# Optimization experiments

Hardware: AMD Instinct MI355X
Metric: run time of the kernel (lower is better)

## Reference

```python
import jax, jax.numpy as jnp
import numpy as np

DIM = 768
NUM_HEADS = 16
D_K = DIM // NUM_HEADS


def setup_inputs() -> dict:
    key = jax.random.key(0)
    ks = jax.random.split(key, 9)
    B, T = 4, 2048
    s = 1.0 / np.sqrt(DIM)
    return {
        "x": jax.random.normal(ks[0], (B, T, DIM), dtype=jnp.float32),
        "Wq": jax.random.normal(ks[1], (DIM, DIM), dtype=jnp.float32) * s,
        "bq": jnp.zeros((DIM,), dtype=jnp.float32),
        "Wk": jax.random.normal(ks[2], (DIM, DIM), dtype=jnp.float32) * s,
        "bk": jnp.zeros((DIM,), dtype=jnp.float32),
        "Wv": jax.random.normal(ks[3], (DIM, DIM), dtype=jnp.float32) * s,
        "bv": jnp.zeros((DIM,), dtype=jnp.float32),
        "Wp": jax.random.normal(ks[4], (DIM, DIM), dtype=jnp.float32) * s,
        "bp": jnp.zeros((DIM,), dtype=jnp.float32),
    }


def reference(x, Wq, bq, Wk, bk, Wv, bv, Wp, bp):
    B, T, _ = x.shape
    # QKV projections (weights stored as [in, out])
    q = x @ Wq + bq
    k = x @ Wk + bk
    v = x @ Wv + bv
    # split heads: (B, H, T, d_k)
    q = q.reshape(B, T, NUM_HEADS, D_K).transpose(0, 2, 1, 3)
    k = k.reshape(B, T, NUM_HEADS, D_K).transpose(0, 2, 1, 3)
    v = v.reshape(B, T, NUM_HEADS, D_K).transpose(0, 2, 1, 3)
    # scaled dot-product attention; dropout omitted (eval mode)
    scores = jnp.einsum("bhtd,bhsd->bhts", q, k) / jnp.sqrt(jnp.float32(D_K))
    attn = jax.nn.softmax(scores, axis=-1)
    out = jnp.einsum("bhts,bhsd->bhtd", attn, v)
    out = out.transpose(0, 2, 1, 3).reshape(B, T, DIM)
    return out @ Wp + bp
```

## Files before the change

kernel.cpp:

```cpp
#include <hip/hip_runtime.h>
#include <math.h>

#define T_SEQ 2048
#define B_SZ  4
#define DIM   768
#define NH    16
#define DK    48
#define NQK   1536
#define N3    2304

typedef __bf16 bf16x8 __attribute__((ext_vector_type(8)));
typedef float  f32x4  __attribute__((ext_vector_type(4)));

__device__ __forceinline__ unsigned short f32_to_bf16(float f) {
    unsigned u = __float_as_uint(f);
    u += 0x7FFFu + ((u >> 16) & 1u);
    return (unsigned short)(u >> 16);
}
__device__ __forceinline__ unsigned pack_bf16x2(float a, float b) {
    unsigned r;
    asm("v_cvt_pk_bf16_f32 %0, %1, %2" : "=v"(r) : "v"(a), "v"(b));
    return r;
}
__device__ __forceinline__ void lds_dma16(const unsigned short* g, unsigned short* l) {
    __builtin_amdgcn_global_load_lds(
        (const __attribute__((address_space(1))) unsigned int*)g,
        (__attribute__((address_space(3))) unsigned int*)l, 16, 0, 0);
}

__global__ __launch_bounds__(256) void cvt_x_kernel(
    const float* __restrict__ x, unsigned short* __restrict__ xb)
{
    int i = blockIdx.x * 256 + threadIdx.x;
    const float* p = x + (size_t)i * 8;
    float4 f0 = *(const float4*)p;
    float4 f1 = *(const float4*)(p + 4);
    uint4 u;
    u.x = pack_bf16x2(f0.x, f0.y);
    u.y = pack_bf16x2(f0.z, f0.w);
    u.z = pack_bf16x2(f1.x, f1.y);
    u.w = pack_bf16x2(f1.z, f1.w);
    *(uint4*)(xb + (size_t)i * 8) = u;
}

__global__ __launch_bounds__(256) void pack_w_kernel(
    const float* __restrict__ Wq, const float* __restrict__ Wk,
    const float* __restrict__ Wv, const float* __restrict__ Wp,
    unsigned short* __restrict__ Wt, unsigned short* __restrict__ Wpt,
    float qscale)
{
    __shared__ float T[32][33];
    const int mode = blockIdx.z;
    const float* W = (mode == 0) ? Wq : (mode == 1) ? Wk : (mode == 2) ? Wv : Wp;
    const float sc = (mode == 0) ? qscale : 1.0f;
    const int k0 = blockIdx.x * 32, c0 = blockIdx.y * 32;
    const int tx = threadIdx.x & 31, ty = threadIdx.x >> 5;

#pragma unroll
    for (int r = 0; r < 4; ++r) {
        int row = ty + r * 8;
        T[row][tx] = W[(size_t)(k0 + row) * DIM + c0 + tx];
    }
    __syncthreads();
#pragma unroll
    for (int r = 0; r < 4; ++r) {
        int j   = ty + r * 8;
        int col = c0 + j;
        int k   = k0 + tx;
        unsigned short v = f32_to_bf16(T[tx][j] * sc);
        if (mode < 3) Wt[(size_t)(mode * 768 + col) * DIM + k] = v;
        else          Wpt[(size_t)col * DIM + k] = v;
    }
}

__global__ __launch_bounds__(256) void pack_bias_kernel(
    const float* __restrict__ bq, const float* __restrict__ bk,
    const float* __restrict__ bv, float* __restrict__ b3, float qscale)
{
    int n = blockIdx.x * 256 + threadIdx.x;
    if (n >= N3) return;
    float v;
    if (n < 768)       v = bq[n] * qscale;
    else if (n < 1536) v = bk[n - 768];
    else               v = bv[n - 1536];
    b3[n] = v;
}

__global__ __launch_bounds__(256) void gemm_qkv_kernel(
    const unsigned short* __restrict__ A, const unsigned short* __restrict__ Bt,
    const float* __restrict__ bias, unsigned short* __restrict__ QK,
    unsigned short* __restrict__ vT)
{
    __shared__ __align__(16) unsigned short As[2 * 128 * 32];
    __shared__ __align__(16) unsigned short Bs[2 * 128 * 32];

    const int t = threadIdx.x;
    const int w = t >> 6, lane = t & 63, quad = lane >> 4, lr = lane & 15;
    const int wm = w >> 1, wn = w & 1;

    const int bid = blockIdx.x;
    const int gy8 = bid / 144;
    const int rem = bid - gy8 * 144;
    const int bx  = rem >> 3;
    const int by  = (rem & 7) | (gy8 << 3);
    const int m0 = by * 128, n0 = bx * 128;

    const int cw0 = w * 128, cw1 = w * 128 + 64;
    const int ca = cw0 + lane, cb = cw1 + lane;
    const int ra = ca >> 2, sa = (ca & 3) * 8;
    const int rb = cb >> 2, sb = (cb & 3) * 8;

    const unsigned short* Ara = A  + (size_t)(m0 + ra) * DIM + sa;
    const unsigned short* Arb = A  + (size_t)(m0 + rb) * DIM + sb;
    const unsigned short* Bra = Bt + (size_t)(n0 + ra) * DIM + sa;
    const unsigned short* Brb = Bt + (size_t)(n0 + rb) * DIM + sb;

    f32x4 acc[4][4] = {};

    lds_dma16(Ara, As + cw0 * 8);
    lds_dma16(Arb, As + cw1 * 8);
    lds_dma16(Bra, Bs + cw0 * 8);
    lds_dma16(Brb, Bs + cw1 * 8);
    __syncthreads();

    for (int k0 = 0; k0 < DIM; k0 += 32) {
        const int cur = (k0 >> 5) & 1, nxt = cur ^ 1;
        if (k0 + 32 < DIM) {
            lds_dma16(Ara + k0 + 32, As + nxt * 4096 + cw0 * 8);
            lds_dma16(Arb + k0 + 32, As + nxt * 4096 + cw1 * 8);
            lds_dma16(Bra + k0 + 32, Bs + nxt * 4096 + cw0 * 8);
            lds_dma16(Brb + k0 + 32, Bs + nxt * 4096 + cw1 * 8);
        }
        const unsigned short* Ac = As + cur * 4096;
        const unsigned short* Bc = Bs + cur * 4096;

        bf16x8 af[4], bfr[4];
#pragma unroll
        for (int mt = 0; mt < 4; ++mt)
            af[mt] = *(const bf16x8*)&Ac[(wm * 64 + mt * 16 + lr) * 32 + quad * 8];
#pragma unroll
        for (int nt = 0; nt < 4; ++nt)
            bfr[nt] = *(const bf16x8*)&Bc[(wn * 64 + nt * 16 + lr) * 32 + quad * 8];
        __builtin_amdgcn_s_setprio(1);
#pragma unroll
        for (int mt = 0; mt < 4; ++mt)
#pragma unroll
            for (int nt = 0; nt < 4; ++nt)
                acc[mt][nt] = __builtin_amdgcn_mfma_f32_16x16x32_bf16(
                    af[mt], bfr[nt], acc[mt][nt], 0, 0, 0);
        __builtin_amdgcn_s_setprio(0);
        __syncthreads();
    }

    if (bx < 12) {
#pragma unroll
        for (int nt = 0; nt < 4; ++nt) {
            int col = n0 + wn * 64 + nt * 16 + lr;
            float bv = bias[col];
#pragma unroll
            for (int mt = 0; mt < 4; ++mt)
#pragma unroll
                for (int r = 0; r < 4; ++r) {
                    int row = m0 + wm * 64 + mt * 16 + quad * 4 + r;
                    QK[(size_t)row * NQK + col] = f32_to_bf16(acc[mt][nt][r] + bv);
                }
        }
    } else {
        const int bidx = m0 >> 11;
        const int ts_base = (m0 & 2047) + wm * 64;
#pragma unroll
        for (int nt = 0; nt < 4; ++nt) {
            int col = n0 + wn * 64 + nt * 16 + lr;
            int vcol = col - 1536;
            int hh = vcol / 48, cc = vcol - hh * 48;
            float bv = bias[col];
            unsigned short* dst0 = vT + ((size_t)(bidx * 16 + hh) * 48 + cc) * T_SEQ;
#pragma unroll
            for (int mt = 0; mt < 4; ++mt) {
                int ts = ts_base + mt * 16 + quad * 4;
                uint2 u;
                u.x = pack_bf16x2(acc[mt][nt][0] + bv, acc[mt][nt][1] + bv);
                u.y = pack_bf16x2(acc[mt][nt][2] + bv, acc[mt][nt][3] + bv);
                *(uint2*)(dst0 + ts) = u;
            }
        }
    }
}

__global__ __launch_bounds__(256) void gemm_out_kernel(
    const unsigned short* __restrict__ A, const unsigned short* __restrict__ Bt,
    const float* __restrict__ bias, float* __restrict__ C)
{
    __shared__ __align__(16) unsigned short As[2 * 128 * 32];
    __shared__ __align__(16) unsigned short Bs[2 * 128 * 32];

    const int t = threadIdx.x;
    const int w = t >> 6, lane = t & 63, quad = lane >> 4, lr = lane & 15;
    const int wm = w >> 1, wn = w & 1;
    const int m0 = blockIdx.y * 128, n0 = blockIdx.x * 128;

    const int cw0 = w * 128, cw1 = w * 128 + 64;
    const int ca = cw0 + lane, cb = cw1 + lane;
    const int ra = ca >> 2, sa = (ca & 3) * 8;
    const int rb = cb >> 2, sb = (cb & 3) * 8;

    const unsigned short* Ara = A  + (size_t)(m0 + ra) * DIM + sa;
    const unsigned short* Arb = A  + (size_t)(m0 + rb) * DIM + sb;
    const unsigned short* Bra = Bt + (size_t)(n0 + ra) * DIM + sa;
    const unsigned short* Brb = Bt + (size_t)(n0 + rb) * DIM + sb;

    f32x4 acc[4][4] = {};

    lds_dma16(Ara, As + cw0 * 8);
    lds_dma16(Arb, As + cw1 * 8);
    lds_dma16(Bra, Bs + cw0 * 8);
    lds_dma16(Brb, Bs + cw1 * 8);
    __syncthreads();

    for (int k0 = 0; k0 < DIM; k0 += 32) {
        const int cur = (k0 >> 5) & 1, nxt = cur ^ 1;
        if (k0 + 32 < DIM) {
            lds_dma16(Ara + k0 + 32, As + nxt * 4096 + cw0 * 8);
            lds_dma16(Arb + k0 + 32, As + nxt * 4096 + cw1 * 8);
            lds_dma16(Bra + k0 + 32, Bs + nxt * 4096 + cw0 * 8);
            lds_dma16(Brb + k0 + 32, Bs + nxt * 4096 + cw1 * 8);
        }
        const unsigned short* Ac = As + cur * 4096;
        const unsigned short* Bc = Bs + cur * 4096;

        bf16x8 af[4], bfr[4];
#pragma unroll
        for (int mt = 0; mt < 4; ++mt)
            af[mt] = *(const bf16x8*)&Ac[(wm * 64 + mt * 16 + lr) * 32 + quad * 8];
#pragma unroll
        for (int nt = 0; nt < 4; ++nt)
            bfr[nt] = *(const bf16x8*)&Bc[(wn * 64 + nt * 16 + lr) * 32 + quad * 8];
        __builtin_amdgcn_s_setprio(1);
#pragma unroll
        for (int mt = 0; mt < 4; ++mt)
#pragma unroll
            for (int nt = 0; nt < 4; ++nt)
                acc[mt][nt] = __builtin_amdgcn_mfma_f32_16x16x32_bf16(
                    af[mt], bfr[nt], acc[mt][nt], 0, 0, 0);
        __builtin_amdgcn_s_setprio(0);
        __syncthreads();
    }

#pragma unroll
    for (int nt = 0; nt < 4; ++nt) {
        int col = n0 + wn * 64 + nt * 16 + lr;
        float bv = bias[col];
#pragma unroll
        for (int mt = 0; mt < 4; ++mt)
#pragma unroll
            for (int r = 0; r < 4; ++r) {
                int row = m0 + wm * 64 + mt * 16 + quad * 4 + r;
                C[(size_t)row * DIM + col] = acc[mt][nt][r] + bv;
            }
    }
}

__global__ __launch_bounds__(256, 4) void attn_kernel(
    const unsigned short* __restrict__ QK, const unsigned short* __restrict__ vT,
    unsigned short* __restrict__ Ob)
{
    __shared__ __align__(16) unsigned short Ks[2 * 64 * 48];
    __shared__ __align__(16) unsigned short Vt[2 * 48 * 64];
    __shared__ __align__(16) unsigned short Ps[4 * 32 * 64];

    const int t = threadIdx.x;
    const int w = t >> 6, lane = t & 63, quad = lane >> 4, lr = lane & 15;

    const int bid = blockIdx.x;
    const int qt = (bid >> 3) & 15;
    const int g  = (bid & 7) | ((bid >> 7) << 3);
    const int h  = g & 15;
    const int b  = g >> 4;

    const int base = b * T_SEQ, q0 = qt * 128;
    const int hq = h * DK, hk = 768 + h * DK;
    const int qrow = base + q0 + w * 32;
    const int psw = lr & 7;

    bf16x8 qa[2], qb[2];
#pragma unroll
    for (int mt = 0; mt < 2; ++mt) {
        const unsigned short* qp = QK + (size_t)(qrow + mt * 16 + lr) * NQK + hq;
        qa[mt] = *(const bf16x8*)(qp + quad * 8);
        qb[mt] = *(const bf16x8*)(qp + 32 + quad * 8);
    }

    const unsigned short* gp[3];
    unsigned short*       lp0[3];
    int                   gstep[3];
#pragma unroll
    for (int i = 0; i < 3; ++i) {
        int c = w * 3 + i;
        if (c < 6) {
            int e = c * 512 + lane * 8;
            int r = e / 48, col = e - r * 48;
            gp[i]    = QK + (size_t)(base + r) * NQK + hk + col;
            lp0[i]   = Ks + c * 512;
            gstep[i] = 64 * NQK;
        } else {
            int cc = c - 6;
            int e = cc * 512 + lane * 8;
            int d = e >> 6, p = (e >> 3) & 7;
            int key = (p ^ (d & 7)) * 8;
            gp[i]    = vT + ((size_t)(b * NH + h) * DK + d) * T_SEQ + key;
            lp0[i]   = Vt + cc * 512;
            gstep[i] = 64;
        }
    }

    lds_dma16(gp[0], lp0[0]); gp[0] += gstep[0];
    lds_dma16(gp[1], lp0[1]); gp[1] += gstep[1];
    lds_dma16(gp[2], lp0[2]); gp[2] += gstep[2];
    __syncthreads();

    f32x4 Oacc[2][3] = {};
    float l_acc[2] = {0.0f, 0.0f};
    unsigned short* Pw = Ps + (w * 32) * 64;

    for (int kt = 0; kt < T_SEQ / 64; ++kt) {
        const int cur = kt & 1, nxt = cur ^ 1;
        if (kt + 1 < T_SEQ / 64) {
            lds_dma16(gp[0], lp0[0] + nxt * 3072); gp[0] += gstep[0];
            lds_dma16(gp[1], lp0[1] + nxt * 3072); gp[1] += gstep[1];
            lds_dma16(gp[2], lp0[2] + nxt * 3072); gp[2] += gstep[2];
        }
        const unsigned short* Kc = Ks + cur * 3072;
        const unsigned short* Vc = Vt + cur * 3072;

        {
            bf16x8 ka[4], kb[4];
#pragma unroll
            for (int nt = 0; nt < 4; ++nt)
                ka[nt] = *(const bf16x8*)(Kc + (nt * 16 + lr) * 48 + quad * 8);
            if (quad < 2) {
#pragma unroll
                for (int nt = 0; nt < 4; ++nt)
                    kb[nt] = *(const bf16x8*)(Kc + (nt * 16 + lr) * 48 + 32 + quad * 8);
            } else {
                bf16x8 z = {};
#pragma unroll
                for (int nt = 0; nt < 4; ++nt) kb[nt] = z;
            }
#pragma unroll
            for (int mt = 0; mt < 2; ++mt) {
                float rs = 0.0f;
#pragma unroll
                for (int nt = 0; nt < 4; ++nt) {
                    f32x4 st = {};
                    __builtin_amdgcn_s_setprio(1);
                    st = __builtin_amdgcn_mfma_f32_16x16x32_bf16(ka[nt], qa[mt], st, 0, 0, 0);
                    st = __builtin_amdgcn_mfma_f32_16x16x32_bf16(kb[nt], qb[mt], st, 0, 0, 0);
                    __builtin_amdgcn_s_setprio(0);
                    float p0 = __builtin_amdgcn_exp2f(st[0]);
                    float p1 = __builtin_amdgcn_exp2f(st[1]);
                    float p2 = __builtin_amdgcn_exp2f(st[2]);
                    float p3 = __builtin_amdgcn_exp2f(st[3]);
                    rs += (p0 + p1) + (p2 + p3);
                    uint2 pk;
                    pk.x = pack_bf16x2(p0, p1);
                    pk.y = pack_bf16x2(p2, p3);
                    int eo = nt * 16 + quad * 4;
                    int es = (((eo >> 3) ^ psw) << 3) | (eo & 7);
                    *(uint2*)&Pw[(mt * 16 + lr) * 64 + es] = pk;
                }
                rs += __shfl_xor(rs, 16);
                rs += __shfl_xor(rs, 32);
                l_acc[mt] += rs;
            }
        }

        {
            bf16x8 aP[2][2];
#pragma unroll
            for (int mt = 0; mt < 2; ++mt) {
                aP[mt][0] = *(const bf16x8*)&Pw[(mt * 16 + lr) * 64 + ((quad ^ psw) * 8)];
                aP[mt][1] = *(const bf16x8*)&Pw[(mt * 16 + lr) * 64 + (((4 + quad) ^ psw) * 8)];
            }
            __builtin_amdgcn_s_setprio(1);
#pragma unroll
            for (int on = 0; on < 3; ++on) {
                const unsigned short* vp = Vc + (on * 16 + lr) * 64;
                bf16x8 v0 = *(const bf16x8*)(vp + ((quad ^ psw) * 8));
                bf16x8 v1 = *(const bf16x8*)(vp + (((4 + quad) ^ psw) * 8));
#pragma unroll
                for (int mt = 0; mt < 2; ++mt) {
                    Oacc[mt][on] = __builtin_amdgcn_mfma_f32_16x16x32_bf16(
                        aP[mt][0], v0, Oacc[mt][on], 0, 0, 0);
                    Oacc[mt][on] = __builtin_amdgcn_mfma_f32_16x16x32_bf16(
                        aP[mt][1], v1, Oacc[mt][on], 0, 0, 0);
                }
            }
            __builtin_amdgcn_s_setprio(0);
        }
        __syncthreads();
    }

#pragma unroll
    for (int mt = 0; mt < 2; ++mt) {
#pragma unroll
        for (int r = 0; r < 4; ++r) {
            float l = __shfl(l_acc[mt], quad * 4 + r);
            float inv = 1.0f / l;
            int row = qrow + mt * 16 + quad * 4 + r;
#pragma unroll
            for (int on = 0; on < 3; ++on)
                Ob[(size_t)row * DIM + h * DK + on * 16 + lr] =
                    f32_to_bf16(Oacc[mt][on][r] * inv);
        }
    }
}

extern "C" void kernel_launch(void* const* d_in, const int* in_sizes, int n_in,
                              void* d_out, int out_size, void* d_ws, size_t ws_size,
                              hipStream_t stream) {
    (void)in_sizes; (void)n_in; (void)out_size; (void)ws_size;

    const float* x  = (const float*)d_in[0];
    const float* Wq = (const float*)d_in[1];
    const float* bq = (const float*)d_in[2];
    const float* Wk = (const float*)d_in[3];
    const float* bk = (const float*)d_in[4];
    const float* Wv = (const float*)d_in[5];
    const float* bv = (const float*)d_in[6];
    const float* Wp = (const float*)d_in[7];
    const float* bp = (const float*)d_in[8];
    float* out = (float*)d_out;

    const size_t M = (size_t)B_SZ * T_SEQ;

    char* ws = (char*)d_ws;
    unsigned short* xb  = (unsigned short*)ws;  ws += M * DIM * 2;
    unsigned short* qk  = (unsigned short*)ws;  ws += M * NQK * 2;
    unsigned short* vT  = (unsigned short*)ws;  ws += M * DIM * 2;
    unsigned short* aob = (unsigned short*)ws;  ws += M * DIM * 2;
    unsigned short* Wt  = (unsigned short*)ws;  ws += (size_t)N3 * DIM * 2;
    unsigned short* Wpt = (unsigned short*)ws;  ws += (size_t)DIM * DIM * 2;
    float*          b3  = (float*)ws;           ws += N3 * 4;

    const float qscale = 0.14433756729740643f * 1.4426950408889634f;

    cvt_x_kernel<<<dim3((int)(M * DIM / 8 / 256)), 256, 0, stream>>>(x, xb);
    pack_w_kernel<<<dim3(DIM / 32, DIM / 32, 4), 256, 0, stream>>>(
        Wq, Wk, Wv, Wp, Wt, Wpt, qscale);
    pack_bias_kernel<<<dim3((N3 + 255) / 256), 256, 0, stream>>>(bq, bk, bv, b3, qscale);

    gemm_qkv_kernel<<<dim3(1152), 256, 0, stream>>>(xb, Wt, b3, qk, vT);

    attn_kernel<<<dim3(1024), 256, 0, stream>>>(qk, vT, aob);

    gemm_out_kernel<<<dim3(DIM / 128, (int)(M / 128)), 256, 0, stream>>>(
        aob, Wpt, bp, out);
}
```

Before: 271.0 us.

## Use partial vmcnt waits with raw barriers to keep prefetch in flight

Replaces the __syncthreads at each K-loop step in both GEMMs and the attention kernel with an explicit s_waitcnt vmcnt(N) plus s_barrier. The wait covers only the current buffer's DMA loads, so the next tile's prefetch can stay in flight across the barrier. The attention kernel also drops its s_setprio hints and switches from a swizzled 1D block-index mapping to a plain 3D grid, which changes the order blocks are scheduled in and may affect L2 reuse. The correctness of the hand-written vmcnt counts depends on the compiler not emitting other vector memory ops in between.

```diff
diff --git a/kernel.cpp b/kernel.cpp
--- a/kernel.cpp
+++ b/kernel.cpp
@@ -121,7 +121,6 @@
     lds_dma16(Arb, As + cw1 * 8);
     lds_dma16(Bra, Bs + cw0 * 8);
     lds_dma16(Brb, Bs + cw1 * 8);
-    __syncthreads();
 
     for (int k0 = 0; k0 < DIM; k0 += 32) {
         const int cur = (k0 >> 5) & 1, nxt = cur ^ 1;
@@ -130,7 +129,13 @@
             lds_dma16(Arb + k0 + 32, As + nxt * 4096 + cw1 * 8);
             lds_dma16(Bra + k0 + 32, Bs + nxt * 4096 + cw0 * 8);
             lds_dma16(Brb + k0 + 32, Bs + nxt * 4096 + cw1 * 8);
-        }
+            asm volatile("s_waitcnt vmcnt(4)" ::: "memory");
+        } else {
+            asm volatile("s_waitcnt vmcnt(0)" ::: "memory");
+        }
+        __builtin_amdgcn_s_barrier();
+        __builtin_amdgcn_sched_barrier(0);
+
         const unsigned short* Ac = As + cur * 4096;
         const unsigned short* Bc = Bs + cur * 4096;
 
@@ -149,7 +154,7 @@
                 acc[mt][nt] = __builtin_amdgcn_mfma_f32_16x16x32_bf16(
                     af[mt], bfr[nt], acc[mt][nt], 0, 0, 0);
         __builtin_amdgcn_s_setprio(0);
-        __syncthreads();
+        __builtin_amdgcn_s_barrier();
     }
 
     if (bx < 12) {
@@ -215,7 +220,6 @@
     lds_dma16(Arb, As + cw1 * 8);
     lds_dma16(Bra, Bs + cw0 * 8);
     lds_dma16(Brb, Bs + cw1 * 8);
-    __syncthreads();
 
     for (int k0 = 0; k0 < DIM; k0 += 32) {
         const int cur = (k0 >> 5) & 1, nxt = cur ^ 1;
@@ -224,7 +228,13 @@
             lds_dma16(Arb + k0 + 32, As + nxt * 4096 + cw1 * 8);
             lds_dma16(Bra + k0 + 32, Bs + nxt * 4096 + cw0 * 8);
             lds_dma16(Brb + k0 + 32, Bs + nxt * 4096 + cw1 * 8);
-        }
+            asm volatile("s_waitcnt vmcnt(4)" ::: "memory");
+        } else {
+            asm volatile("s_waitcnt vmcnt(0)" ::: "memory");
+        }
+        __builtin_amdgcn_s_barrier();
+        __builtin_amdgcn_sched_barrier(0);
+
         const unsigned short* Ac = As + cur * 4096;
         const unsigned short* Bc = Bs + cur * 4096;
 
@@ -243,7 +253,7 @@
                 acc[mt][nt] = __builtin_amdgcn_mfma_f32_16x16x32_bf16(
                     af[mt], bfr[nt], acc[mt][nt], 0, 0, 0);
         __builtin_amdgcn_s_setprio(0);
-        __syncthreads();
+        __builtin_amdgcn_s_barrier();
     }
 
 #pragma unroll
@@ -270,13 +280,7 @@
 
     const int t = threadIdx.x;
     const int w = t >> 6, lane = t & 63, quad = lane >> 4, lr = lane & 15;
-
-    const int bid = blockIdx.x;
-    const int qt = (bid >> 3) & 15;
-    const int g  = (bid & 7) | ((bid >> 7) << 3);
-    const int h  = g & 15;
-    const int b  = g >> 4;
-
+    const int qt = blockIdx.x, h = blockIdx.y, b = blockIdx.z;
     const int base = b * T_SEQ, q0 = qt * 128;
     const int hq = h * DK, hk = 768 + h * DK;
     const int qrow = base + q0 + w * 32;
@@ -316,7 +320,6 @@
     lds_dma16(gp[0], lp0[0]); gp[0] += gstep[0];
     lds_dma16(gp[1], lp0[1]); gp[1] += gstep[1];
     lds_dma16(gp[2], lp0[2]); gp[2] += gstep[2];
-    __syncthreads();
 
     f32x4 Oacc[2][3] = {};
     float l_acc[2] = {0.0f, 0.0f};
@@ -328,7 +331,13 @@
             lds_dma16(gp[0], lp0[0] + nxt * 3072); gp[0] += gstep[0];
             lds_dma16(gp[1], lp0[1] + nxt * 3072); gp[1] += gstep[1];
             lds_dma16(gp[2], lp0[2] + nxt * 3072); gp[2] += gstep[2];
-        }
+            asm volatile("s_waitcnt vmcnt(3)" ::: "memory");
+        } else {
+            asm volatile("s_waitcnt vmcnt(0)" ::: "memory");
+        }
+        __builtin_amdgcn_s_barrier();
+        __builtin_amdgcn_sched_barrier(0);
+
         const unsigned short* Kc = Ks + cur * 3072;
         const unsigned short* Vc = Vt + cur * 3072;
 
@@ -352,10 +361,8 @@
 #pragma unroll
                 for (int nt = 0; nt < 4; ++nt) {
                     f32x4 st = {};
-                    __builtin_amdgcn_s_setprio(1);
                     st = __builtin_amdgcn_mfma_f32_16x16x32_bf16(ka[nt], qa[mt], st, 0, 0, 0);
                     st = __builtin_amdgcn_mfma_f32_16x16x32_bf16(kb[nt], qb[mt], st, 0, 0, 0);
-                    __builtin_amdgcn_s_setprio(0);
                     float p0 = __builtin_amdgcn_exp2f(st[0]);
                     float p1 = __builtin_amdgcn_exp2f(st[1]);
                     float p2 = __builtin_amdgcn_exp2f(st[2]);
@@ -381,7 +388,6 @@
                 aP[mt][0] = *(const bf16x8*)&Pw[(mt * 16 + lr) * 64 + ((quad ^ psw) * 8)];
                 aP[mt][1] = *(const bf16x8*)&Pw[(mt * 16 + lr) * 64 + (((4 + quad) ^ psw) * 8)];
             }
-            __builtin_amdgcn_s_setprio(1);
 #pragma unroll
             for (int on = 0; on < 3; ++on) {
                 const unsigned short* vp = Vc + (on * 16 + lr) * 64;
@@ -395,9 +401,8 @@
                         aP[mt][1], v1, Oacc[mt][on], 0, 0, 0);
                 }
             }
-            __builtin_amdgcn_s_setprio(0);
-        }
-        __syncthreads();
+        }
+        __builtin_amdgcn_s_barrier();
     }
 
 #pragma unroll
@@ -451,7 +456,7 @@
 
     gemm_qkv_kernel<<<dim3(1152), 256, 0, stream>>>(xb, Wt, b3, qk, vT);
 
-    attn_kernel<<<dim3(1024), 256, 0, stream>>>(qk, vT, aob);
+    attn_kernel<<<dim3(T_SEQ / 128, NH, B_SZ), 256, 0, stream>>>(qk, vT, aob);
 
     gemm_out_kernel<<<dim3(DIM / 128, (int)(M / 128)), 256, 0, stream>>>(
         aob, Wpt, bp, out);
```

Result: faster. 245.9 us (-9.3%).
